# Optimization experiments

Measured on AMD Instinct MI355X. Metric: run time of the kernel, lower is better.

Reference implementation:

```python
import jax, jax.numpy as jnp
import numpy as np
import math

HIDDEN = 1024
N_HEADS = 16
HEAD_DIM = HIDDEN // N_HEADS
N_BLOCKS = 16
BATCH = 2
SEQ = 4096


def setup_inputs() -> dict:
    key = jax.random.key(0)
    ks = jax.random.split(key, 8)
    attention_input = jax.random.normal(ks[0], (BATCH, SEQ, HIDDEN), dtype=jnp.float32)
    attention_mask = jnp.ones((BATCH, SEQ), dtype=jnp.float32)
    # permutation over the num_blocks*num_heads flattened (block, head) axis
    permutation = jax.random.permutation(ks[1], N_BLOCKS * N_HEADS)
    init = 0.02
    q_w = jax.random.normal(ks[2], (HIDDEN, N_HEADS, HEAD_DIM), dtype=jnp.float32) * init
    q_b = jax.random.normal(ks[3], (N_HEADS, HEAD_DIM), dtype=jnp.float32) * init
    k_w = jax.random.normal(ks[4], (HIDDEN, N_HEADS, HEAD_DIM), dtype=jnp.float32) * init
    k_b = jax.random.normal(ks[5], (N_HEADS, HEAD_DIM), dtype=jnp.float32) * init
    v_w = jax.random.normal(ks[6], (HIDDEN, N_HEADS, HEAD_DIM), dtype=jnp.float32) * init
    v_b = jax.random.normal(ks[7], (N_HEADS, HEAD_DIM), dtype=jnp.float32) * init
    return {"attention_input": attention_input, "attention_mask": attention_mask,
            "permutation": permutation, "q_w": q_w, "q_b": q_b,
            "k_w": k_w, "k_b": k_b, "v_w": v_w, "v_b": v_b}


def reference(attention_input, attention_mask, permutation, q_w, q_b, k_w, k_b, v_w, v_b):
    B = attention_mask.shape[0]
    S = attention_mask.shape[1]
    nb = N_BLOCKS
    nh, d = q_b.shape
    blk = S // nb
    # QKV projections: [B,S,H] x [H,N,D] -> [B,S,N,D]
    q = jnp.einsum('bsh,hnd->bsnd', attention_input, q_w) + q_b
    k = jnp.einsum('bsh,hnd->bsnd', attention_input, k_w) + k_b
    v = jnp.einsum('bsh,hnd->bsnd', attention_input, v_w) + v_b

    def blockify(x):  # [B,S,N,D] -> [B, nb, nh, blk, d]
        return x.reshape(B, nb, blk, nh, d).transpose(0, 1, 3, 2, 4)

    q = blockify(q)
    # flatten (block, head) axis and gather per permutation
    k = blockify(k).reshape(B, nb * nh, blk, d)[:, permutation].reshape(B, nb, nh, blk, d)
    v = blockify(v).reshape(B, nb * nh, blk, d)[:, permutation].reshape(B, nb, nh, blk, d)

    scale = 1.0 / math.sqrt(float(d))
    logits = jnp.einsum('bgnqd,bgnkd->bgnqk', q, k) * scale  # block-local scores
    attn = jax.nn.softmax(logits, axis=-1)  # dropout prob 0 / eval mode
    ctx = jnp.einsum('bgnqk,bgnkd->bgnqd', attn, v)
    # [B,nb,nh,blk,d] -> [B,nb,blk,nh,d] -> [B,S,nh,d]
    return ctx.transpose(0, 1, 3, 2, 4).reshape(B, S, nh, d)
```

## Files before the change

### kernel.cpp

```cpp
#include <hip/hip_runtime.h>
#include <hip/hip_bf16.h>
#include <stdint.h>

typedef __attribute__((ext_vector_type(4))) float f32x4;
typedef __attribute__((ext_vector_type(8))) short s16x8;

__device__ inline short f2bf(float f) {
  union { float f; uint32_t u; } v; v.f = f;
  uint32_t r = v.u + 0x7fffu + ((v.u >> 16) & 1u);
  return (short)(r >> 16);
}

__device__ inline void gload_lds16(const void* g, void* l) {
  __builtin_amdgcn_global_load_lds((const __attribute__((address_space(1))) void*)g,
                                   (__attribute__((address_space(3))) void*)l,
                                   16, 0, 0);
}

#define MFMA16 __builtin_amdgcn_mfma_f32_16x16x32_bf16

__global__ __launch_bounds__(256) void k_convert_x(const float* __restrict__ x,
                                                   short* __restrict__ xb) {
  int i = (blockIdx.x * 256 + threadIdx.x) * 8;
  const float4* p = (const float4*)(x + i);
  float4 a = p[0], b = p[1];
  s16x8 o;
  o[0] = f2bf(a.x); o[1] = f2bf(a.y); o[2] = f2bf(a.z); o[3] = f2bf(a.w);
  o[4] = f2bf(b.x); o[5] = f2bf(b.y); o[6] = f2bf(b.z); o[7] = f2bf(b.w);
  *(s16x8*)(xb + i) = o;
}

__global__ __launch_bounds__(256) void k_transpose_w(const float* __restrict__ qw,
                                                     const float* __restrict__ kw,
                                                     const float* __restrict__ vw,
                                                     short* __restrict__ wt) {
  __shared__ float tile[64][65];
  int a  = blockIdx.x >> 8;
  int t2 = blockIdx.x & 255;
  int k0 = (t2 >> 4) << 6;
  int n0 = (t2 & 15) << 6;
  const float* w = (a == 0) ? qw : (a == 1) ? kw : vw;
  int c = threadIdx.x & 63, rr = threadIdx.x >> 6;
#pragma unroll
  for (int i = 0; i < 16; ++i) {
    int r = i * 4 + rr;
    tile[r][c] = w[(k0 + r) * 1024 + n0 + c];
  }
  __syncthreads();
  short* o = wt + a * 1048576;
#pragma unroll
  for (int i = 0; i < 16; ++i) {
    int r = i * 4 + rr;
    o[(n0 + r) * 1024 + k0 + c] = f2bf(tile[c][r]);
  }
}

__global__ __launch_bounds__(256, 2) void k_gemm(const short* __restrict__ xb,
                                                 const short* __restrict__ wt,
                                                 const float* __restrict__ qbias,
                                                 const float* __restrict__ kbias,
                                                 const float* __restrict__ vbias,
                                                 short* __restrict__ Qo,
                                                 short* __restrict__ Ko,
                                                 short* __restrict__ Vo) {
  __shared__ short lds[36864];
  const int tid = threadIdx.x, lane = tid & 63, wv = tid >> 6;
  const int wm = wv >> 1, wn = wv & 1;
  const int mt = blockIdx.x, by = blockIdx.y;
  const int a = by >> 3;
  const short* asrc = xb + (size_t)(mt * 256) * 1024;
  const short* bsrc = wt + (size_t)a * 1048576 + (size_t)((by & 7) * 128) * 1024;

  int srcA[4], dstA[4], srcB[2], dstB[2];
#pragma unroll
  for (int i = 0; i < 4; ++i) {
    int L = i * 256 + tid, s = L & 31;
    int row = (L >> 5) * 8 + (s >> 2);
    int c = (s & 3) ^ ((s >> 3) & 3);
    srcA[i] = row * 1024 + c * 8;
    dstA[i] = L * 16;
  }
#pragma unroll
  for (int i = 0; i < 2; ++i) {
    int L = i * 256 + tid, s = L & 31;
    int row = (L >> 5) * 8 + (s >> 2);
    int c = (s & 3) ^ ((s >> 3) & 3);
    srcB[i] = row * 1024 + c * 8;
    dstB[i] = 16384 + L * 16;
  }

  int aoff[8], boff[4];
#pragma unroll
  for (int m = 0; m < 8; ++m) {
    int row = wm * 128 + m * 16 + (lane & 15);
    aoff[m] = ((row >> 3) * 32 + (row & 7) * 4 + ((lane >> 4) ^ ((row >> 1) & 3))) * 16;
  }
#pragma unroll
  for (int n = 0; n < 4; ++n) {
    int row = wn * 64 + n * 16 + (lane & 15);
    boff[n] = 16384 + ((row >> 3) * 32 + (row & 7) * 4 + ((lane >> 4) ^ ((row >> 1) & 3))) * 16;
  }

  f32x4 acc[8][4] = {};

  auto STAGE = [&](int t, int bb) {
    const short* at = asrc + t * 32;
    const short* bt = bsrc + t * 32;
    char* l = (char*)lds + bb;
#pragma unroll
    for (int i = 0; i < 4; ++i) gload_lds16(at + srcA[i], l + dstA[i]);
#pragma unroll
    for (int i = 0; i < 2; ++i) gload_lds16(bt + srcB[i], l + dstB[i]);
  };

  STAGE(0, 0);
  STAGE(1, 24576);
  int bcur = 0, bpre = 49152;

  for (int t = 0; t < 31; ++t) {
    asm volatile("s_waitcnt vmcnt(6)" ::: "memory");
    __builtin_amdgcn_s_barrier();
    asm volatile("" ::: "memory");
    if (t < 30) STAGE(t + 2, bpre);
    const char* bufc = (const char*)lds + bcur;
    s16x8 af[8], bf[4];
#pragma unroll
    for (int m = 0; m < 8; ++m) af[m] = *(const s16x8*)(bufc + aoff[m]);
#pragma unroll
    for (int n = 0; n < 4; ++n) bf[n] = *(const s16x8*)(bufc + boff[n]);
    __builtin_amdgcn_s_setprio(1);
#pragma unroll
    for (int m = 0; m < 8; ++m)
#pragma unroll
      for (int n = 0; n < 4; ++n)
        acc[m][n] = MFMA16(af[m], bf[n], acc[m][n], 0, 0, 0);
    __builtin_amdgcn_s_setprio(0);
    bcur += 24576; if (bcur == 73728) bcur = 0;
    bpre += 24576; if (bpre == 73728) bpre = 0;
  }
  asm volatile("s_waitcnt vmcnt(0)" ::: "memory");
  __builtin_amdgcn_s_barrier();
  asm volatile("" ::: "memory");
  {
    const char* bufc = (const char*)lds + bcur;
    s16x8 af[8], bf[4];
#pragma unroll
    for (int m = 0; m < 8; ++m) af[m] = *(const s16x8*)(bufc + aoff[m]);
#pragma unroll
    for (int n = 0; n < 4; ++n) bf[n] = *(const s16x8*)(bufc + boff[n]);
    __builtin_amdgcn_s_setprio(1);
#pragma unroll
    for (int m = 0; m < 8; ++m)
#pragma unroll
      for (int n = 0; n < 4; ++n)
        acc[m][n] = MFMA16(af[m], bf[n], acc[m][n], 0, 0, 0);
    __builtin_amdgcn_s_setprio(0);
  }

  const float* bias = (a == 0) ? qbias : (a == 1) ? kbias : vbias;
  short* outp = (a == 0) ? Qo : (a == 1) ? Ko : Vo;
  int nbase = (by & 7) * 128 + wn * 64;
  int mbase = mt * 256 + wm * 128;
#pragma unroll
  for (int n = 0; n < 4; ++n) {
    int nloc = nbase + n * 16 + (lane & 15);
    float bv = bias[nloc];
#pragma unroll
    for (int m = 0; m < 8; ++m)
#pragma unroll
      for (int r = 0; r < 4; ++r) {
        int mm = mbase + m * 16 + ((lane >> 4) << 2) + r;
        outp[(size_t)mm * 1024 + nloc] = f2bf(acc[m][n][r] + bv);
      }
  }
}

__global__ __launch_bounds__(256, 2) void k_attn(const short* __restrict__ Qb,
                                                 const short* __restrict__ Kb,
                                                 const short* __restrict__ Vb,
                                                 const int* __restrict__ perm,
                                                 float* __restrict__ out) {
  __shared__ short Ks[256 * 64];
  __shared__ short Vs[64 * 256];
  __shared__ short QP[8192];

  int tid = threadIdx.x;
  int lane = tid & 63, wv = tid >> 6;
  int bx = blockIdx.x;
  int wg = (bx & 7) * 128 + (bx >> 3);
  int b = wg >> 9, g = (wg >> 5) & 15, n = (wg >> 1) & 15, h = wg & 1;
  int p = perm[g * 16 + n];
  int pg = p >> 4, ph = p & 15;

  const short* qsrc = Qb + (size_t)(b * 4096 + g * 256 + h * 128) * 1024 + n * 64;
  const short* ksrc = Kb + (size_t)(b * 4096 + pg * 256) * 1024 + ph * 64;
  const short* vsrc = Vb + (size_t)(b * 4096 + pg * 256) * 1024 + ph * 64;

  s16x8 vreg[8];
#pragma unroll
  for (int i = 0; i < 8; ++i) {
    int c = i * 256 + tid;
    int t = c >> 3;
    int d0 = (c & 7) << 3;
    vreg[i] = *(const s16x8*)(vsrc + t * 1024 + d0);
  }
#pragma unroll
  for (int i = 0; i < 4; ++i) {
    int c = i * 256 + tid;
    int row = c >> 3;
    int sc = ((c & 7) << 4) ^ ((row & 7) << 4);
    gload_lds16(qsrc + row * 1024 + (sc >> 1), (char*)QP + c * 16);
  }
#pragma unroll
  for (int i = 0; i < 8; ++i) {
    int c = i * 256 + tid;
    int row = c >> 3;
    int sc = ((c & 7) << 4) ^ ((row & 7) << 4);
    gload_lds16(ksrc + row * 1024 + (sc >> 1), (char*)Ks + c * 16);
  }
#pragma unroll
  for (int i = 0; i < 8; ++i) {
    int c = i * 256 + tid;
    int t = c >> 3;
    int d0 = (c & 7) << 3;
#pragma unroll
    for (int j = 0; j < 8; ++j) {
      int d = d0 + j;
      int sl = (d & 7) ^ ((d >> 3) & 7);
      int by = d * 512 + ((t * 2) ^ (sl << 4));
      *(short*)((char*)Vs + by) = vreg[i][j];
    }
  }
  __syncthreads();

  int qr0 = wv * 32;
  f32x4 accS[2][16] = {};
#pragma unroll
  for (int ks = 0; ks < 2; ++ks) {
    int cb = (ks << 6) + ((lane >> 4) << 4);
    s16x8 aq[2];
#pragma unroll
    for (int rf = 0; rf < 2; ++rf) {
      int row = qr0 + rf * 16 + (lane & 15);
      aq[rf] = *(const s16x8*)((const char*)QP + row * 128 + (cb ^ ((row & 7) << 4)));
    }
#pragma unroll
    for (int cf = 0; cf < 16; ++cf) {
      int row = cf * 16 + (lane & 15);
      s16x8 bk = *(const s16x8*)((const char*)Ks + row * 128 + (cb ^ ((row & 7) << 4)));
      accS[0][cf] = MFMA16(aq[0], bk, accS[0][cf], 0, 0, 0);
      accS[1][cf] = MFMA16(aq[1], bk, accS[1][cf], 0, 0, 0);
    }
  }

  const float sc_log2e = 0.125f * 1.44269504088896f;
  float mx[2][4], inv[2][4];
#pragma unroll
  for (int rf = 0; rf < 2; ++rf)
#pragma unroll
    for (int r = 0; r < 4; ++r) {
      float m_ = accS[rf][0][r];
#pragma unroll
      for (int cf = 1; cf < 16; ++cf) m_ = fmaxf(m_, accS[rf][cf][r]);
#pragma unroll
      for (int msk = 1; msk < 16; msk <<= 1) m_ = fmaxf(m_, __shfl_xor(m_, msk));
      mx[rf][r] = m_;
    }
#pragma unroll
  for (int rf = 0; rf < 2; ++rf)
#pragma unroll
    for (int r = 0; r < 4; ++r) {
      float s_ = 0.f;
#pragma unroll
      for (int cf = 0; cf < 16; ++cf) {
        float e = exp2f((accS[rf][cf][r] - mx[rf][r]) * sc_log2e);
        accS[rf][cf][r] = e;
        s_ += e;
      }
#pragma unroll
      for (int msk = 1; msk < 16; msk <<= 1) s_ += __shfl_xor(s_, msk);
      inv[rf][r] = 1.0f / s_;
    }

  __syncthreads();

  f32x4 accO[2][4] = {};
  short* pchunk = QP + wv * 1024;
#pragma unroll
  for (int ks = 0; ks < 8; ++ks) {
#pragma unroll
    for (int rf = 0; rf < 2; ++rf)
#pragma unroll
      for (int half = 0; half < 2; ++half) {
        int cf = ks * 2 + half;
        int kvl = half * 16 + (lane & 15);
        int qp = (lane >> 4) << 2;
        int base = rf * 512 + ((kvl >> 3) << 7) + (kvl & 7);
#pragma unroll
        for (int r = 0; r < 4; ++r)
          pchunk[base + (qp + r) * 8] = f2bf(accS[rf][cf][r]);
      }
    int cbv = (ks << 6) + ((lane >> 4) << 4);
#pragma unroll
    for (int rf = 0; rf < 2; ++rf) {
      s16x8 ap = *(const s16x8*)(pchunk + rf * 512 + lane * 8);
#pragma unroll
      for (int dc = 0; dc < 4; ++dc) {
        int vrow = dc * 16 + (lane & 15);
        int sl = (vrow & 7) ^ ((vrow >> 3) & 7);
        s16x8 bv = *(const s16x8*)((const char*)Vs + vrow * 512 + (cbv ^ (sl << 4)));
        accO[rf][dc] = MFMA16(ap, bv, accO[rf][dc], 0, 0, 0);
      }
    }
  }

#pragma unroll
  for (int rf = 0; rf < 2; ++rf)
#pragma unroll
    for (int dc = 0; dc < 4; ++dc)
#pragma unroll
      for (int r = 0; r < 4; ++r) {
        int q = h * 128 + qr0 + rf * 16 + ((lane >> 4) << 2) + r;
        int d = dc * 16 + (lane & 15);
        out[(size_t)((b * 4096 + g * 256 + q) * 16 + n) * 64 + d] = accO[rf][dc][r] * inv[rf][r];
      }
}

extern "C" void kernel_launch(void* const* d_in, const int* in_sizes, int n_in,
                              void* d_out, int out_size, void* d_ws, size_t ws_size,
                              hipStream_t stream) {
  const float* x    = (const float*)d_in[0];
  const int*   perm = (const int*)d_in[2];
  const float* qw   = (const float*)d_in[3];
  const float* qb   = (const float*)d_in[4];
  const float* kw   = (const float*)d_in[5];
  const float* kb   = (const float*)d_in[6];
  const float* vw   = (const float*)d_in[7];
  const float* vb   = (const float*)d_in[8];
  float* out = (float*)d_out;

  char* ws = (char*)d_ws;
  short* Xb = (short*)(ws);
  short* Wt = (short*)(ws + 16777216UL);
  short* Qb = (short*)(ws + 23068672UL);
  short* Kb = (short*)(ws + 39845888UL);
  short* Vb = (short*)(ws + 56623104UL);

  k_convert_x<<<4096, 256, 0, stream>>>(x, Xb);
  k_transpose_w<<<768, 256, 0, stream>>>(qw, kw, vw, Wt);
  k_gemm<<<dim3(32, 24), 256, 0, stream>>>(Xb, Wt, qb, kb, vb, Qb, Kb, Vb);
  k_attn<<<1024, 256, 0, stream>>>(Qb, Kb, Vb, perm, out);
}
```

Measured before the change: 101.3 us.

## Merge prep kernels and overlap V staging with QK^T in attention

```diff
diff --git a/kernel.cpp b/kernel.cpp
--- a/kernel.cpp
+++ b/kernel.cpp
@@ -19,24 +19,27 @@
 
 #define MFMA16 __builtin_amdgcn_mfma_f32_16x16x32_bf16
 
-__global__ __launch_bounds__(256) void k_convert_x(const float* __restrict__ x,
-                                                   short* __restrict__ xb) {
-  int i = (blockIdx.x * 256 + threadIdx.x) * 8;
-  const float4* p = (const float4*)(x + i);
-  float4 a = p[0], b = p[1];
-  s16x8 o;
-  o[0] = f2bf(a.x); o[1] = f2bf(a.y); o[2] = f2bf(a.z); o[3] = f2bf(a.w);
-  o[4] = f2bf(b.x); o[5] = f2bf(b.y); o[6] = f2bf(b.z); o[7] = f2bf(b.w);
-  *(s16x8*)(xb + i) = o;
-}
-
-__global__ __launch_bounds__(256) void k_transpose_w(const float* __restrict__ qw,
-                                                     const float* __restrict__ kw,
-                                                     const float* __restrict__ vw,
-                                                     short* __restrict__ wt) {
+__global__ __launch_bounds__(256) void k_prep(const float* __restrict__ x,
+                                              short* __restrict__ xb,
+                                              const float* __restrict__ qw,
+                                              const float* __restrict__ kw,
+                                              const float* __restrict__ vw,
+                                              short* __restrict__ wt) {
   __shared__ float tile[64][65];
-  int a  = blockIdx.x >> 8;
-  int t2 = blockIdx.x & 255;
+  int bx = blockIdx.x;
+  if (bx < 4096) {
+    int i = (bx * 256 + threadIdx.x) * 8;
+    const float4* p = (const float4*)(x + i);
+    float4 a = p[0], b = p[1];
+    s16x8 o;
+    o[0] = f2bf(a.x); o[1] = f2bf(a.y); o[2] = f2bf(a.z); o[3] = f2bf(a.w);
+    o[4] = f2bf(b.x); o[5] = f2bf(b.y); o[6] = f2bf(b.z); o[7] = f2bf(b.w);
+    *(s16x8*)(xb + i) = o;
+    return;
+  }
+  bx -= 4096;
+  int a  = bx >> 8;
+  int t2 = bx & 255;
   int k0 = (t2 >> 4) << 6;
   int n0 = (t2 & 15) << 6;
   const float* w = (a == 0) ? qw : (a == 1) ? kw : vw;
@@ -182,7 +185,7 @@
                                                  float* __restrict__ out) {
   __shared__ short Ks[256 * 64];
   __shared__ short Vs[64 * 256];
-  __shared__ short QP[8192];
+  __shared__ short Ps[4 * 1024];
 
   int tid = threadIdx.x;
   int lane = tid & 63, wv = tid >> 6;
@@ -196,6 +199,16 @@
   const short* ksrc = Kb + (size_t)(b * 4096 + pg * 256) * 1024 + ph * 64;
   const short* vsrc = Vb + (size_t)(b * 4096 + pg * 256) * 1024 + ph * 64;
 
+  int qr0 = wv * 32;
+
+#pragma unroll
+  for (int i = 0; i < 8; ++i) {
+    int c = i * 256 + tid;
+    int row = c >> 3;
+    int sc = ((c & 7) << 4) ^ ((row & 7) << 4);
+    gload_lds16(ksrc + row * 1024 + (sc >> 1), (char*)Ks + c * 16);
+  }
+  __builtin_amdgcn_sched_barrier(0);
   s16x8 vreg[8];
 #pragma unroll
   for (int i = 0; i < 8; ++i) {
@@ -204,20 +217,32 @@
     int d0 = (c & 7) << 3;
     vreg[i] = *(const s16x8*)(vsrc + t * 1024 + d0);
   }
-#pragma unroll
-  for (int i = 0; i < 4; ++i) {
-    int c = i * 256 + tid;
-    int row = c >> 3;
-    int sc = ((c & 7) << 4) ^ ((row & 7) << 4);
-    gload_lds16(qsrc + row * 1024 + (sc >> 1), (char*)QP + c * 16);
-  }
-#pragma unroll
-  for (int i = 0; i < 8; ++i) {
-    int c = i * 256 + tid;
-    int row = c >> 3;
-    int sc = ((c & 7) << 4) ^ ((row & 7) << 4);
-    gload_lds16(ksrc + row * 1024 + (sc >> 1), (char*)Ks + c * 16);
-  }
+  s16x8 qreg[2][2];
+#pragma unroll
+  for (int rf = 0; rf < 2; ++rf)
+#pragma unroll
+    for (int ks = 0; ks < 2; ++ks) {
+      int row = qr0 + rf * 16 + (lane & 15);
+      qreg[rf][ks] = *(const s16x8*)(qsrc + row * 1024 + ks * 32 + ((lane >> 4) << 3));
+    }
+  __builtin_amdgcn_sched_barrier(0);
+  asm volatile("s_waitcnt vmcnt(12)" ::: "memory");
+  __builtin_amdgcn_s_barrier();
+  __builtin_amdgcn_sched_barrier(0);
+
+  f32x4 accS[2][16] = {};
+#pragma unroll
+  for (int ks = 0; ks < 2; ++ks) {
+    int cb = (ks << 6) + ((lane >> 4) << 4);
+#pragma unroll
+    for (int cf = 0; cf < 16; ++cf) {
+      int row = cf * 16 + (lane & 15);
+      s16x8 bk = *(const s16x8*)((const char*)Ks + row * 128 + (cb ^ ((row & 7) << 4)));
+      accS[0][cf] = MFMA16(qreg[0][ks], bk, accS[0][cf], 0, 0, 0);
+      accS[1][cf] = MFMA16(qreg[1][ks], bk, accS[1][cf], 0, 0, 0);
+    }
+  }
+
 #pragma unroll
   for (int i = 0; i < 8; ++i) {
     int c = i * 256 + tid;
@@ -233,26 +258,6 @@
   }
   __syncthreads();
 
-  int qr0 = wv * 32;
-  f32x4 accS[2][16] = {};
-#pragma unroll
-  for (int ks = 0; ks < 2; ++ks) {
-    int cb = (ks << 6) + ((lane >> 4) << 4);
-    s16x8 aq[2];
-#pragma unroll
-    for (int rf = 0; rf < 2; ++rf) {
-      int row = qr0 + rf * 16 + (lane & 15);
-      aq[rf] = *(const s16x8*)((const char*)QP + row * 128 + (cb ^ ((row & 7) << 4)));
-    }
-#pragma unroll
-    for (int cf = 0; cf < 16; ++cf) {
-      int row = cf * 16 + (lane & 15);
-      s16x8 bk = *(const s16x8*)((const char*)Ks + row * 128 + (cb ^ ((row & 7) << 4)));
-      accS[0][cf] = MFMA16(aq[0], bk, accS[0][cf], 0, 0, 0);
-      accS[1][cf] = MFMA16(aq[1], bk, accS[1][cf], 0, 0, 0);
-    }
-  }
-
   const float sc_log2e = 0.125f * 1.44269504088896f;
   float mx[2][4], inv[2][4];
 #pragma unroll
@@ -282,10 +287,8 @@
       inv[rf][r] = 1.0f / s_;
     }
 
-  __syncthreads();
-
   f32x4 accO[2][4] = {};
-  short* pchunk = QP + wv * 1024;
+  short* pchunk = Ps + wv * 1024;
 #pragma unroll
   for (int ks = 0; ks < 8; ++ks) {
 #pragma unroll
@@ -346,8 +349,7 @@
   short* Kb = (short*)(ws + 39845888UL);
   short* Vb = (short*)(ws + 56623104UL);
 
-  k_convert_x<<<4096, 256, 0, stream>>>(x, Xb);
-  k_transpose_w<<<768, 256, 0, stream>>>(qw, kw, vw, Wt);
+  k_prep<<<4864, 256, 0, stream>>>(x, Xb, qw, kw, vw, Wt);
   k_gemm<<<dim3(32, 24), 256, 0, stream>>>(Xb, Wt, qb, kb, vb, Qb, Kb, Vb);
   k_attn<<<1024, 256, 0, stream>>>(Qb, Kb, Vb, perm, out);
 }
```

Result: no change. 99.56 us (-1.7%).
